# Kernel optimization log

Hardware: AMD Instinct MI355X
Metric: run time of the kernel (lower is better)

Reference implementation:

```python
import jax, jax.numpy as jnp
import numpy as np

N_USERS = 40000
N_ITEMS = 20000
D = 128
N_EDGES = 320000
LAYERS = 3
EPS = 1e-7
BATCH = 4096


def setup_inputs() -> dict:
    key = jax.random.key(0)
    k1, k2, k3, k4, k5, k6, k7 = jax.random.split(key, 7)
    user_emb = jax.random.normal(k1, (N_USERS, D), jnp.float32) * 0.02
    item_emb = jax.random.normal(k2, (N_ITEMS, D), jnp.float32) * 0.02
    adj_user = jax.random.randint(k3, (N_EDGES,), 0, N_USERS)
    adj_item = jax.random.randint(k4, (N_EDGES,), 0, N_ITEMS)
    user = jax.random.randint(k5, (BATCH,), 0, N_USERS)
    # items are 1-indexed in the original forward (pos_item - 1)
    pos_item = jax.random.randint(k6, (BATCH,), 1, N_ITEMS + 1)
    neg_item = jax.random.randint(k7, (BATCH,), 1, N_ITEMS + 1)
    return dict(user_emb=user_emb, item_emb=item_emb,
                adj_user=adj_user, adj_item=adj_item,
                user=user, pos_item=pos_item, neg_item=neg_item)


def _norm_adj(adj_user, adj_item):
    # Symmetric bipartite adjacency A over (U+I) nodes with D^-1/2 A D^-1/2 norm.
    N = N_USERS + N_ITEMS
    rows = jnp.concatenate([adj_user, adj_item + N_USERS])
    cols = jnp.concatenate([adj_item + N_USERS, adj_user])
    deg = jnp.zeros((N,), jnp.float32).at[rows].add(1.0) + EPS  # (A>0).sum(1)+eps
    dinv = deg ** -0.5
    vals = dinv[rows] * dinv[cols]  # interaction values are 1.0
    return rows, cols, vals


def _encode(user_emb, item_emb, rows, cols, vals):
    N = N_USERS + N_ITEMS
    x = jnp.concatenate([user_emb, item_emb], axis=0)  # [N, D]
    acc = x
    for _ in range(LAYERS):
        # SpMM: out[r] += v_e * x[c] for each edge e=(r,c)
        x = jax.ops.segment_sum(vals[:, None] * x[cols], rows, num_segments=N)
        acc = acc + x
    all_emb = acc / jnp.float32(LAYERS + 1)  # mean over layer outputs
    return all_emb[:N_USERS], all_emb[N_USERS:]


def reference(user_emb, item_emb, adj_user, adj_item, user, pos_item, neg_item):
    rows, cols, vals = _norm_adj(adj_user, adj_item)
    u_lat, i_lat = _encode(user_emb, item_emb, rows, cols, vals)
    tu = u_lat[user]                  # [B, D]
    pi = i_lat[pos_item - 1]          # [B, D]
    ni = i_lat[neg_item - 1]          # [B, D]
    pos_scores = jnp.sum(tu * pi, axis=-1)
    neg_scores = jnp.sum(tu * ni, axis=-1)
    # BPR loss: -mean(log sigmoid(pos - neg))
    loss = -jnp.mean(jax.nn.log_sigmoid(pos_scores - neg_scores))
    return loss
```

## Files before the change

### kernel.cpp

```cpp
#include <hip/hip_runtime.h>
#include <math.h>

#define N_USERS 40000
#define N_ITEMS 20000
#define NNODES  60000
#define D       128
#define N_EDGES 320000
#define NDIR    (2 * N_EDGES)
#define EPS_    1e-7f
#define BATCH   4096
#define STRIDE  64
#define ZSCALE  256.0f
#define BPR_BLOCKS (BATCH / 4)
#define FILL_GRPS  320
#define FILL_BLOCKS (8 * FILL_GRPS)
#define INIT_BLOCKS (NNODES * 16 / 256)

typedef float vf2 __attribute__((ext_vector_type(2)));

__device__ __forceinline__ void add_fp8x8(float* a, uint2 t) {
    vf2 p0 = __builtin_amdgcn_cvt_pk_f32_fp8(t.x, false);
    vf2 p1 = __builtin_amdgcn_cvt_pk_f32_fp8(t.x, true);
    vf2 p2 = __builtin_amdgcn_cvt_pk_f32_fp8(t.y, false);
    vf2 p3 = __builtin_amdgcn_cvt_pk_f32_fp8(t.y, true);
    a[0] += p0.x; a[1] += p0.y; a[2] += p1.x; a[3] += p1.y;
    a[4] += p2.x; a[5] += p2.y; a[6] += p3.x; a[7] += p3.y;
}

__device__ __forceinline__ uint2 pack_fp8x8(const float* vin) {
    float v[8];
    #pragma unroll
    for (int k = 0; k < 8; ++k) v[k] = fminf(fmaxf(vin[k], -448.0f), 448.0f);
    int lo = __builtin_amdgcn_cvt_pk_fp8_f32(v[0], v[1], 0,  false);
    lo     = __builtin_amdgcn_cvt_pk_fp8_f32(v[2], v[3], lo, true);
    int hi = __builtin_amdgcn_cvt_pk_fp8_f32(v[4], v[5], 0,  false);
    hi     = __builtin_amdgcn_cvt_pk_fp8_f32(v[6], v[7], hi, true);
    return make_uint2((unsigned)lo, (unsigned)hi);
}

__global__ void fill_ell(const int* __restrict__ au, const int* __restrict__ ai,
                         int* __restrict__ fillc, int* __restrict__ colell) {
    const int bucket = blockIdx.x & 7;
    const int grp    = blockIdx.x >> 3;
    for (int e = grp * 256 + threadIdx.x; e < N_EDGES; e += FILL_GRPS * 256) {
        int u  = au[e];
        int it = N_USERS + ai[e];
        if (u / 10000 == bucket) {
            int pos = atomicAdd(&fillc[u], 1);
            if (pos < STRIDE) colell[(u << 6) + pos] = it;
        }
        if (4 + (it - N_USERS) / 5000 == bucket) {
            int pos = atomicAdd(&fillc[it], 1);
            if (pos < STRIDE) colell[(it << 6) + pos] = u;
        }
    }
}

__global__ void dinv_and_init(const int* __restrict__ fillc,
                              float* __restrict__ dinv, float* __restrict__ dinv2,
                              const float4* __restrict__ ue, const float4* __restrict__ ie,
                              uint2* __restrict__ z0) {
    int i   = blockIdx.x * 256 + threadIdx.x;
    int row = i >> 4;
    int sub = i & 15;
    float w = rsqrtf((float)fillc[row] + EPS_);
    if (sub == 0) { dinv[row] = w; dinv2[row] = w * w; }
    float4 e0, e1;
    if (row < N_USERS) {
        int b4 = row * 32 + sub * 2;
        e0 = ue[b4]; e1 = ue[b4 + 1];
    } else {
        int b4 = (row - N_USERS) * 32 + sub * 2;
        e0 = ie[b4]; e1 = ie[b4 + 1];
    }
    float ws = w * ZSCALE;
    float v[8] = { e0.x * ws, e0.y * ws, e0.z * ws, e0.w * ws,
                   e1.x * ws, e1.y * ws, e1.z * ws, e1.w * ws };
    z0[i] = pack_fp8x8(v);
}

__global__ void spmm_full(const int* __restrict__ cnt, const int* __restrict__ colell,
                          const float* __restrict__ dinv2,
                          const uint2* __restrict__ z, uint2* __restrict__ znxt) {
    int tid = blockIdx.x * 256 + threadIdx.x;
    int row = tid >> 4;
    int sub = threadIdx.x & 15;
    if (row >= NNODES) return;
    int e = cnt[row];
    const int* rc = colell + (row << 6);
    float a0[8] = {0,0,0,0,0,0,0,0};
    float a1[8] = {0,0,0,0,0,0,0,0};
    int j = 0;
    for (; j + 3 < e; j += 4) {
        int c0 = rc[j], c1 = rc[j + 1], c2 = rc[j + 2], c3 = rc[j + 3];
        uint2 t0 = z[(c0 << 4) + sub];
        uint2 t1 = z[(c1 << 4) + sub];
        uint2 t2 = z[(c2 << 4) + sub];
        uint2 t3 = z[(c3 << 4) + sub];
        add_fp8x8(a0, t0); add_fp8x8(a1, t1);
        add_fp8x8(a0, t2); add_fp8x8(a1, t3);
    }
    for (; j < e; ++j) {
        uint2 t0 = z[(rc[j] << 4) + sub];
        add_fp8x8(a0, t0);
    }
    float w = dinv2[row];
    float v[8];
    #pragma unroll
    for (int k = 0; k < 8; ++k) v[k] = w * (a0[k] + a1[k]);
    znxt[(row << 4) + sub] = pack_fp8x8(v);
}

__global__ void bpr_loss(const float4* __restrict__ ue, const float4* __restrict__ ie,
                         const uint2* __restrict__ z1, const uint2* __restrict__ z2,
                         const float* __restrict__ dinv, const float* __restrict__ dinv2,
                         const int* __restrict__ cnt, const int* __restrict__ colell,
                         const int* __restrict__ user, const int* __restrict__ pos,
                         const int* __restrict__ neg,
                         float* __restrict__ lacc, int* __restrict__ done,
                         float* __restrict__ out) {
    __shared__ float s[4];
    int gw   = (blockIdx.x * 256 + threadIdx.x) >> 6;
    int lane = threadIdx.x & 63;
    int sub  = lane & 15;
    int q    = lane >> 4;
    int u = user[gw];
    int p = N_USERS + pos[gw] - 1;
    int n = N_USERS + neg[gw] - 1;
    int node = (q == 1) ? p : (q == 2) ? n : u;
    float vals[8] = {0,0,0,0,0,0,0,0};
    if (q < 3) {
        float4 e0, e1;
        if (node < N_USERS) {
            int b4 = node * 32 + sub * 2;
            e0 = ue[b4]; e1 = ue[b4 + 1];
        } else {
            int b4 = (node - N_USERS) * 32 + sub * 2;
            e0 = ie[b4]; e1 = ie[b4 + 1];
        }
        float w0 = dinv[node] * ZSCALE;
        vals[0] = w0 * e0.x; vals[1] = w0 * e0.y;
        vals[2] = w0 * e0.z; vals[3] = w0 * e0.w;
        vals[4] = w0 * e1.x; vals[5] = w0 * e1.y;
        vals[6] = w0 * e1.z; vals[7] = w0 * e1.w;
        int o = (node << 4) + sub;
        add_fp8x8(vals, z1[o]);
        add_fp8x8(vals, z2[o]);
        int e = cnt[node];
        const int* rc = colell + (node << 6);
        float a0[8] = {0,0,0,0,0,0,0,0};
        float a1[8] = {0,0,0,0,0,0,0,0};
        int j = 0;
        for (; j + 3 < e; j += 4) {
            int c0 = rc[j], c1 = rc[j + 1], c2 = rc[j + 2], c3 = rc[j + 3];
            uint2 t0 = z2[(c0 << 4) + sub];
            uint2 t1 = z2[(c1 << 4) + sub];
            uint2 t2 = z2[(c2 << 4) + sub];
            uint2 t3 = z2[(c3 << 4) + sub];
            add_fp8x8(a0, t0); add_fp8x8(a1, t1);
            add_fp8x8(a0, t2); add_fp8x8(a1, t3);
        }
        for (; j < e; ++j) {
            uint2 t0 = z2[(rc[j] << 4) + sub];
            add_fp8x8(a0, t0);
        }
        float w = dinv2[node];
        #pragma unroll
        for (int k = 0; k < 8; ++k) vals[k] += w * (a0[k] + a1[k]);
    }
    float dotp = 0.0f;
    #pragma unroll
    for (int k = 0; k < 8; ++k) {
        float av = __shfl(vals[k], sub);
        dotp += av * vals[k];
    }
    #pragma unroll
    for (int off = 8; off; off >>= 1) dotp += __shfl_down(dotp, off, 16);
    float sp = __shfl(dotp, 16);
    float sn = __shfl(dotp, 32);
    if (lane == 0) {
        float du = dinv[u], dp = dinv[p], dn = dinv[n];
        const float inv = 1.0f / (16.0f * ZSCALE * ZSCALE);
        float diff = (sp / (du * dp) - sn / (du * dn)) * inv;
        s[threadIdx.x >> 6] = fminf(diff, 0.0f) - log1pf(expf(-fabsf(diff)));
    }
    __syncthreads();
    if (threadIdx.x == 0) {
        atomicAdd(lacc, s[0] + s[1] + s[2] + s[3]);
        __threadfence();
        int prev = atomicAdd(done, 1);
        if (prev == BPR_BLOCKS - 1) {
            float total = atomicAdd(lacc, 0.0f);
            out[0] = -total * (1.0f / (float)BATCH);
        }
    }
}

extern "C" void kernel_launch(void* const* d_in, const int* in_sizes, int n_in,
                              void* d_out, int out_size, void* d_ws, size_t ws_size,
                              hipStream_t stream) {
    const float* ue  = (const float*)d_in[0];
    const float* ie  = (const float*)d_in[1];
    const int*   au  = (const int*)d_in[2];
    const int*   ai  = (const int*)d_in[3];
    const int*   usr = (const int*)d_in[4];
    const int*   pos = (const int*)d_in[5];
    const int*   neg = (const int*)d_in[6];
    float*       out = (float*)d_out;

    const size_t ZNQ = (size_t)NNODES * 16;

    uint2* z0     = (uint2*)d_ws;
    uint2* z1     = z0 + ZNQ;
    uint2* z2     = z1 + ZNQ;
    float* dinv   = (float*)(z2 + ZNQ);
    float* dinv2  = dinv + NNODES;
    int*   fillc  = (int*)(dinv2 + NNODES);
    float* lacc   = (float*)(fillc + NNODES);
    int*   done   = (int*)(lacc + 1);
    int*   colell = (int*)(lacc + 4);

    hipMemsetAsync(fillc, 0, (NNODES + 4) * sizeof(int), stream);

    fill_ell<<<FILL_BLOCKS, 256, 0, stream>>>(au, ai, fillc, colell);
    dinv_and_init<<<INIT_BLOCKS, 256, 0, stream>>>(fillc, dinv, dinv2,
                                                   (const float4*)ue,
                                                   (const float4*)ie, z0);

    const int FULL_BLOCKS = (NNODES + 15) / 16;
    spmm_full<<<FULL_BLOCKS, 256, 0, stream>>>(fillc, colell, dinv2, z0, z1);
    spmm_full<<<FULL_BLOCKS, 256, 0, stream>>>(fillc, colell, dinv2, z1, z2);

    bpr_loss<<<BPR_BLOCKS, 256, 0, stream>>>((const float4*)ue, (const float4*)ie,
                                             z1, z2, dinv, dinv2, fillc, colell,
                                             usr, pos, neg, lacc, done, out);
}
```

Baseline: 185.9 us.

## Widen per-thread fp8 gathers to 16 bytes and drop dinv arrays

Each thread in the SpMM and BPR kernels now handles 16 fp8 values (a uint4 load) instead of 8, so each row is covered by 8 lanes rather than 16. This doubles bytes per gather instruction and halves the threads per row. The dinv/dinv2 arrays are removed and the weights are recomputed from the edge counts. The edge-list fill loads edges two at a time as int2. The aim is fewer memory instructions and less global traffic, at the cost of more registers per thread and possibly lower occupancy.

```diff
diff --git a/kernel.cpp b/kernel.cpp
--- a/kernel.cpp
+++ b/kernel.cpp
@@ -6,65 +6,86 @@
 #define NNODES  60000
 #define D       128
 #define N_EDGES 320000
-#define NDIR    (2 * N_EDGES)
 #define EPS_    1e-7f
 #define BATCH   4096
 #define STRIDE  64
 #define ZSCALE  256.0f
-#define BPR_BLOCKS (BATCH / 4)
+#define BPR_BLOCKS (BATCH / 8)
 #define FILL_GRPS  320
 #define FILL_BLOCKS (8 * FILL_GRPS)
 #define INIT_BLOCKS (NNODES * 16 / 256)
+#define FULL_BLOCKS (NNODES * 8 / 256)
 
 typedef float vf2 __attribute__((ext_vector_type(2)));
 
-__device__ __forceinline__ void add_fp8x8(float* a, uint2 t) {
+__device__ __forceinline__ void add_fp8x16(float* a, uint4 t) {
     vf2 p0 = __builtin_amdgcn_cvt_pk_f32_fp8(t.x, false);
     vf2 p1 = __builtin_amdgcn_cvt_pk_f32_fp8(t.x, true);
     vf2 p2 = __builtin_amdgcn_cvt_pk_f32_fp8(t.y, false);
     vf2 p3 = __builtin_amdgcn_cvt_pk_f32_fp8(t.y, true);
-    a[0] += p0.x; a[1] += p0.y; a[2] += p1.x; a[3] += p1.y;
-    a[4] += p2.x; a[5] += p2.y; a[6] += p3.x; a[7] += p3.y;
-}
-
-__device__ __forceinline__ uint2 pack_fp8x8(const float* vin) {
-    float v[8];
-    #pragma unroll
-    for (int k = 0; k < 8; ++k) v[k] = fminf(fmaxf(vin[k], -448.0f), 448.0f);
-    int lo = __builtin_amdgcn_cvt_pk_fp8_f32(v[0], v[1], 0,  false);
-    lo     = __builtin_amdgcn_cvt_pk_fp8_f32(v[2], v[3], lo, true);
-    int hi = __builtin_amdgcn_cvt_pk_fp8_f32(v[4], v[5], 0,  false);
-    hi     = __builtin_amdgcn_cvt_pk_fp8_f32(v[6], v[7], hi, true);
-    return make_uint2((unsigned)lo, (unsigned)hi);
-}
-
-__global__ void fill_ell(const int* __restrict__ au, const int* __restrict__ ai,
+    vf2 p4 = __builtin_amdgcn_cvt_pk_f32_fp8(t.z, false);
+    vf2 p5 = __builtin_amdgcn_cvt_pk_f32_fp8(t.z, true);
+    vf2 p6 = __builtin_amdgcn_cvt_pk_f32_fp8(t.w, false);
+    vf2 p7 = __builtin_amdgcn_cvt_pk_f32_fp8(t.w, true);
+    a[0]  += p0.x; a[1]  += p0.y; a[2]  += p1.x; a[3]  += p1.y;
+    a[4]  += p2.x; a[5]  += p2.y; a[6]  += p3.x; a[7]  += p3.y;
+    a[8]  += p4.x; a[9]  += p4.y; a[10] += p5.x; a[11] += p5.y;
+    a[12] += p6.x; a[13] += p6.y; a[14] += p7.x; a[15] += p7.y;
+}
+
+__device__ __forceinline__ uint4 pack_fp8x16(const float* vin) {
+    float v[16];
+    #pragma unroll
+    for (int k = 0; k < 16; ++k) v[k] = fminf(fmaxf(vin[k], -448.0f), 448.0f);
+    int w0 = __builtin_amdgcn_cvt_pk_fp8_f32(v[0],  v[1],  0,  false);
+    w0     = __builtin_amdgcn_cvt_pk_fp8_f32(v[2],  v[3],  w0, true);
+    int w1 = __builtin_amdgcn_cvt_pk_fp8_f32(v[4],  v[5],  0,  false);
+    w1     = __builtin_amdgcn_cvt_pk_fp8_f32(v[6],  v[7],  w1, true);
+    int w2 = __builtin_amdgcn_cvt_pk_fp8_f32(v[8],  v[9],  0,  false);
+    w2     = __builtin_amdgcn_cvt_pk_fp8_f32(v[10], v[11], w2, true);
+    int w3 = __builtin_amdgcn_cvt_pk_fp8_f32(v[12], v[13], 0,  false);
+    w3     = __builtin_amdgcn_cvt_pk_fp8_f32(v[14], v[15], w3, true);
+    uint4 o; o.x = (unsigned)w0; o.y = (unsigned)w1;
+    o.z = (unsigned)w2; o.w = (unsigned)w3;
+    return o;
+}
+
+__global__ void fill_ell(const int2* __restrict__ au2, const int2* __restrict__ ai2,
                          int* __restrict__ fillc, int* __restrict__ colell) {
     const int bucket = blockIdx.x & 7;
     const int grp    = blockIdx.x >> 3;
-    for (int e = grp * 256 + threadIdx.x; e < N_EDGES; e += FILL_GRPS * 256) {
-        int u  = au[e];
-        int it = N_USERS + ai[e];
-        if (u / 10000 == bucket) {
-            int pos = atomicAdd(&fillc[u], 1);
-            if (pos < STRIDE) colell[(u << 6) + pos] = it;
-        }
-        if (4 + (it - N_USERS) / 5000 == bucket) {
-            int pos = atomicAdd(&fillc[it], 1);
-            if (pos < STRIDE) colell[(it << 6) + pos] = u;
-        }
-    }
-}
-
-__global__ void dinv_and_init(const int* __restrict__ fillc,
-                              float* __restrict__ dinv, float* __restrict__ dinv2,
-                              const float4* __restrict__ ue, const float4* __restrict__ ie,
-                              uint2* __restrict__ z0) {
+    const int NE2    = N_EDGES / 2;
+    for (int i = grp * 256 + threadIdx.x; i < NE2; i += FILL_GRPS * 256) {
+        int2 us = au2[i];
+        int2 is = ai2[i];
+        int u0 = us.x, i0 = N_USERS + is.x;
+        int u1 = us.y, i1 = N_USERS + is.y;
+        if (u0 / 10000 == bucket) {
+            int pos = atomicAdd(&fillc[u0], 1);
+            if (pos < STRIDE) colell[(u0 << 6) + pos] = i0;
+        }
+        if (u1 / 10000 == bucket) {
+            int pos = atomicAdd(&fillc[u1], 1);
+            if (pos < STRIDE) colell[(u1 << 6) + pos] = i1;
+        }
+        if (4 + (i0 - N_USERS) / 5000 == bucket) {
+            int pos = atomicAdd(&fillc[i0], 1);
+            if (pos < STRIDE) colell[(i0 << 6) + pos] = u0;
+        }
+        if (4 + (i1 - N_USERS) / 5000 == bucket) {
+            int pos = atomicAdd(&fillc[i1], 1);
+            if (pos < STRIDE) colell[(i1 << 6) + pos] = u1;
+        }
+    }
+}
+
+__global__ void init_z(const int* __restrict__ fillc,
+                       const float4* __restrict__ ue, const float4* __restrict__ ie,
+                       uint2* __restrict__ z0) {
     int i   = blockIdx.x * 256 + threadIdx.x;
     int row = i >> 4;
     int sub = i & 15;
-    float w = rsqrtf((float)fillc[row] + EPS_);
-    if (sub == 0) { dinv[row] = w; dinv2[row] = w * w; }
+    float w = rsqrtf((float)fillc[row] + EPS_) * ZSCALE;
     float4 e0, e1;
     if (row < N_USERS) {
         int b4 = row * 32 + sub * 2;
@@ -73,120 +94,131 @@
         int b4 = (row - N_USERS) * 32 + sub * 2;
         e0 = ie[b4]; e1 = ie[b4 + 1];
     }
-    float ws = w * ZSCALE;
-    float v[8] = { e0.x * ws, e0.y * ws, e0.z * ws, e0.w * ws,
-                   e1.x * ws, e1.y * ws, e1.z * ws, e1.w * ws };
-    z0[i] = pack_fp8x8(v);
+    float v[8] = { e0.x * w, e0.y * w, e0.z * w, e0.w * w,
+                   e1.x * w, e1.y * w, e1.z * w, e1.w * w };
+    float c[8];
+    #pragma unroll
+    for (int k = 0; k < 8; ++k) c[k] = fminf(fmaxf(v[k], -448.0f), 448.0f);
+    int lo = __builtin_amdgcn_cvt_pk_fp8_f32(c[0], c[1], 0,  false);
+    lo     = __builtin_amdgcn_cvt_pk_fp8_f32(c[2], c[3], lo, true);
+    int hi = __builtin_amdgcn_cvt_pk_fp8_f32(c[4], c[5], 0,  false);
+    hi     = __builtin_amdgcn_cvt_pk_fp8_f32(c[6], c[7], hi, true);
+    z0[i] = make_uint2((unsigned)lo, (unsigned)hi);
 }
 
 __global__ void spmm_full(const int* __restrict__ cnt, const int* __restrict__ colell,
-                          const float* __restrict__ dinv2,
-                          const uint2* __restrict__ z, uint2* __restrict__ znxt) {
+                          const uint4* __restrict__ z, uint4* __restrict__ znxt) {
     int tid = blockIdx.x * 256 + threadIdx.x;
-    int row = tid >> 4;
-    int sub = threadIdx.x & 15;
-    if (row >= NNODES) return;
+    int row = tid >> 3;
+    int sub = threadIdx.x & 7;
     int e = cnt[row];
     const int* rc = colell + (row << 6);
-    float a0[8] = {0,0,0,0,0,0,0,0};
-    float a1[8] = {0,0,0,0,0,0,0,0};
+    float a0[16], a1[16];
+    #pragma unroll
+    for (int k = 0; k < 16; ++k) { a0[k] = 0.f; a1[k] = 0.f; }
     int j = 0;
     for (; j + 3 < e; j += 4) {
         int c0 = rc[j], c1 = rc[j + 1], c2 = rc[j + 2], c3 = rc[j + 3];
-        uint2 t0 = z[(c0 << 4) + sub];
-        uint2 t1 = z[(c1 << 4) + sub];
-        uint2 t2 = z[(c2 << 4) + sub];
-        uint2 t3 = z[(c3 << 4) + sub];
-        add_fp8x8(a0, t0); add_fp8x8(a1, t1);
-        add_fp8x8(a0, t2); add_fp8x8(a1, t3);
+        uint4 t0 = z[(c0 << 3) + sub];
+        uint4 t1 = z[(c1 << 3) + sub];
+        uint4 t2 = z[(c2 << 3) + sub];
+        uint4 t3 = z[(c3 << 3) + sub];
+        add_fp8x16(a0, t0); add_fp8x16(a1, t1);
+        add_fp8x16(a0, t2); add_fp8x16(a1, t3);
     }
     for (; j < e; ++j) {
-        uint2 t0 = z[(rc[j] << 4) + sub];
-        add_fp8x8(a0, t0);
-    }
-    float w = dinv2[row];
-    float v[8];
-    #pragma unroll
-    for (int k = 0; k < 8; ++k) v[k] = w * (a0[k] + a1[k]);
-    znxt[(row << 4) + sub] = pack_fp8x8(v);
+        uint4 t0 = z[(rc[j] << 3) + sub];
+        add_fp8x16(a0, t0);
+    }
+    float w = 1.0f / ((float)e + EPS_);
+    float v[16];
+    #pragma unroll
+    for (int k = 0; k < 16; ++k) v[k] = w * (a0[k] + a1[k]);
+    znxt[(row << 3) + sub] = pack_fp8x16(v);
 }
 
 __global__ void bpr_loss(const float4* __restrict__ ue, const float4* __restrict__ ie,
-                         const uint2* __restrict__ z1, const uint2* __restrict__ z2,
-                         const float* __restrict__ dinv, const float* __restrict__ dinv2,
+                         const uint4* __restrict__ z1, const uint4* __restrict__ z2,
                          const int* __restrict__ cnt, const int* __restrict__ colell,
                          const int* __restrict__ user, const int* __restrict__ pos,
                          const int* __restrict__ neg,
                          float* __restrict__ lacc, int* __restrict__ done,
                          float* __restrict__ out) {
-    __shared__ float s[4];
-    int gw   = (blockIdx.x * 256 + threadIdx.x) >> 6;
+    __shared__ float s[8];
+    int wave = (blockIdx.x * 256 + threadIdx.x) >> 6;
     int lane = threadIdx.x & 63;
-    int sub  = lane & 15;
-    int q    = lane >> 4;
-    int u = user[gw];
-    int p = N_USERS + pos[gw] - 1;
-    int n = N_USERS + neg[gw] - 1;
-    int node = (q == 1) ? p : (q == 2) ? n : u;
-    float vals[8] = {0,0,0,0,0,0,0,0};
-    if (q < 3) {
-        float4 e0, e1;
-        if (node < N_USERS) {
-            int b4 = node * 32 + sub * 2;
-            e0 = ue[b4]; e1 = ue[b4 + 1];
-        } else {
-            int b4 = (node - N_USERS) * 32 + sub * 2;
-            e0 = ie[b4]; e1 = ie[b4 + 1];
-        }
-        float w0 = dinv[node] * ZSCALE;
-        vals[0] = w0 * e0.x; vals[1] = w0 * e0.y;
-        vals[2] = w0 * e0.z; vals[3] = w0 * e0.w;
-        vals[4] = w0 * e1.x; vals[5] = w0 * e1.y;
-        vals[6] = w0 * e1.z; vals[7] = w0 * e1.w;
-        int o = (node << 4) + sub;
-        add_fp8x8(vals, z1[o]);
-        add_fp8x8(vals, z2[o]);
+    int sg   = lane >> 3;
+    int sub  = lane & 7;
+    int half = sg >> 2;
+    int sgl  = sg & 3;
+    int el   = wave * 2 + half;
+    int u = user[el];
+    int p = N_USERS + pos[el] - 1;
+    int n = N_USERS + neg[el] - 1;
+    int node = (sgl == 1) ? p : (sgl == 2) ? n : u;
+    float cnode = 0.0f;
+    float vals[16];
+    #pragma unroll
+    for (int k = 0; k < 16; ++k) vals[k] = 0.0f;
+    if (sgl < 3) {
         int e = cnt[node];
+        cnode = (float)e;
+        const float4* eb = (node < N_USERS) ? ue : ie;
+        int b4 = ((node < N_USERS) ? node : node - N_USERS) * 32 + sub * 4;
+        float4 e0 = eb[b4], e1 = eb[b4 + 1], e2 = eb[b4 + 2], e3 = eb[b4 + 3];
+        float w0 = rsqrtf(cnode + EPS_) * ZSCALE;
+        vals[0]  = w0 * e0.x; vals[1]  = w0 * e0.y; vals[2]  = w0 * e0.z; vals[3]  = w0 * e0.w;
+        vals[4]  = w0 * e1.x; vals[5]  = w0 * e1.y; vals[6]  = w0 * e1.z; vals[7]  = w0 * e1.w;
+        vals[8]  = w0 * e2.x; vals[9]  = w0 * e2.y; vals[10] = w0 * e2.z; vals[11] = w0 * e2.w;
+        vals[12] = w0 * e3.x; vals[13] = w0 * e3.y; vals[14] = w0 * e3.z; vals[15] = w0 * e3.w;
+        int o = (node << 3) + sub;
+        add_fp8x16(vals, z1[o]);
+        add_fp8x16(vals, z2[o]);
         const int* rc = colell + (node << 6);
-        float a0[8] = {0,0,0,0,0,0,0,0};
-        float a1[8] = {0,0,0,0,0,0,0,0};
+        float a0[16], a1[16];
+        #pragma unroll
+        for (int k = 0; k < 16; ++k) { a0[k] = 0.f; a1[k] = 0.f; }
         int j = 0;
         for (; j + 3 < e; j += 4) {
             int c0 = rc[j], c1 = rc[j + 1], c2 = rc[j + 2], c3 = rc[j + 3];
-            uint2 t0 = z2[(c0 << 4) + sub];
-            uint2 t1 = z2[(c1 << 4) + sub];
-            uint2 t2 = z2[(c2 << 4) + sub];
-            uint2 t3 = z2[(c3 << 4) + sub];
-            add_fp8x8(a0, t0); add_fp8x8(a1, t1);
-            add_fp8x8(a0, t2); add_fp8x8(a1, t3);
+            uint4 t0 = z2[(c0 << 3) + sub];
+            uint4 t1 = z2[(c1 << 3) + sub];
+            uint4 t2 = z2[(c2 << 3) + sub];
+            uint4 t3 = z2[(c3 << 3) + sub];
+            add_fp8x16(a0, t0); add_fp8x16(a1, t1);
+            add_fp8x16(a0, t2); add_fp8x16(a1, t3);
         }
         for (; j < e; ++j) {
-            uint2 t0 = z2[(rc[j] << 4) + sub];
-            add_fp8x8(a0, t0);
-        }
-        float w = dinv2[node];
+            uint4 t0 = z2[(rc[j] << 3) + sub];
+            add_fp8x16(a0, t0);
+        }
+        float w2 = 1.0f / (cnode + EPS_);
         #pragma unroll
-        for (int k = 0; k < 8; ++k) vals[k] += w * (a0[k] + a1[k]);
-    }
+        for (int k = 0; k < 16; ++k) vals[k] += w2 * (a0[k] + a1[k]);
+    }
+    int usrc = sub | (lane & 32);
     float dotp = 0.0f;
     #pragma unroll
-    for (int k = 0; k < 8; ++k) {
-        float av = __shfl(vals[k], sub);
-        dotp += av * vals[k];
-    }
-    #pragma unroll
-    for (int off = 8; off; off >>= 1) dotp += __shfl_down(dotp, off, 16);
-    float sp = __shfl(dotp, 16);
-    float sn = __shfl(dotp, 32);
-    if (lane == 0) {
-        float du = dinv[u], dp = dinv[p], dn = dinv[n];
+    for (int k = 0; k < 16; ++k) dotp += __shfl(vals[k], usrc) * vals[k];
+    dotp += __shfl_down(dotp, 4, 8);
+    dotp += __shfl_down(dotp, 2, 8);
+    dotp += __shfl_down(dotp, 1, 8);
+    float sp = __shfl(dotp, (lane & 32) + 8);
+    float sn = __shfl(dotp, (lane & 32) + 16);
+    float cu = __shfl(cnode, (lane & 32) + 0);
+    float cp = __shfl(cnode, (lane & 32) + 8);
+    float cn = __shfl(cnode, (lane & 32) + 16);
+    if ((lane & 31) == 0) {
+        float du = rsqrtf(cu + EPS_), dp = rsqrtf(cp + EPS_), dn = rsqrtf(cn + EPS_);
         const float inv = 1.0f / (16.0f * ZSCALE * ZSCALE);
         float diff = (sp / (du * dp) - sn / (du * dn)) * inv;
-        s[threadIdx.x >> 6] = fminf(diff, 0.0f) - log1pf(expf(-fabsf(diff)));
+        s[(threadIdx.x >> 6) * 2 + half] =
+            fminf(diff, 0.0f) - log1pf(expf(-fabsf(diff)));
     }
     __syncthreads();
     if (threadIdx.x == 0) {
-        atomicAdd(lacc, s[0] + s[1] + s[2] + s[3]);
+        float t = s[0] + s[1] + s[2] + s[3] + s[4] + s[5] + s[6] + s[7];
+        atomicAdd(lacc, t);
         __threadfence();
         int prev = atomicAdd(done, 1);
         if (prev == BPR_BLOCKS - 1) {
@@ -208,30 +240,27 @@
     const int*   neg = (const int*)d_in[6];
     float*       out = (float*)d_out;
 
-    const size_t ZNQ = (size_t)NNODES * 16;
-
-    uint2* z0     = (uint2*)d_ws;
-    uint2* z1     = z0 + ZNQ;
-    uint2* z2     = z1 + ZNQ;
-    float* dinv   = (float*)(z2 + ZNQ);
-    float* dinv2  = dinv + NNODES;
-    int*   fillc  = (int*)(dinv2 + NNODES);
+    const size_t ZQ4 = (size_t)NNODES * 8;
+
+    uint4* z0     = (uint4*)d_ws;
+    uint4* z1     = z0 + ZQ4;
+    uint4* z2     = z1 + ZQ4;
+    int*   fillc  = (int*)(z2 + ZQ4);
     float* lacc   = (float*)(fillc + NNODES);
     int*   done   = (int*)(lacc + 1);
     int*   colell = (int*)(lacc + 4);
 
     hipMemsetAsync(fillc, 0, (NNODES + 4) * sizeof(int), stream);
 
-    fill_ell<<<FILL_BLOCKS, 256, 0, stream>>>(au, ai, fillc, colell);
-    dinv_and_init<<<INIT_BLOCKS, 256, 0, stream>>>(fillc, dinv, dinv2,
-                                                   (const float4*)ue,
-                                                   (const float4*)ie, z0);
-
-    const int FULL_BLOCKS = (NNODES + 15) / 16;
-    spmm_full<<<FULL_BLOCKS, 256, 0, stream>>>(fillc, colell, dinv2, z0, z1);
-    spmm_full<<<FULL_BLOCKS, 256, 0, stream>>>(fillc, colell, dinv2, z1, z2);
+    fill_ell<<<FILL_BLOCKS, 256, 0, stream>>>((const int2*)au, (const int2*)ai,
+                                              fillc, colell);
+    init_z<<<INIT_BLOCKS, 256, 0, stream>>>(fillc, (const float4*)ue,
+                                            (const float4*)ie, (uint2*)z0);
+
+    spmm_full<<<FULL_BLOCKS, 256, 0, stream>>>(fillc, colell, z0, z1);
+    spmm_full<<<FULL_BLOCKS, 256, 0, stream>>>(fillc, colell, z1, z2);
 
     bpr_loss<<<BPR_BLOCKS, 256, 0, stream>>>((const float4*)ue, (const float4*)ie,
-                                             z1, z2, dinv, dinv2, fillc, colell,
+                                             z1, z2, fillc, colell,
                                              usr, pos, neg, lacc, done, out);
 }
```

Measured after the change: 171.9 us. -7.5%, faster.
